# Optimization experiments

Hardware: AMD Instinct MI355X
Metric: run time of the kernel (lower is better)

## Reference

```python
import jax, jax.numpy as jnp
import numpy as np

DIM, HEADS, RANK = 768, 12, 64
HEAD_DIM = DIM // HEADS

def _xavier(key, shape):
    fan_in, fan_out = shape[1], shape[0]
    std = (2.0 / (fan_in + fan_out)) ** 0.5
    return std * jax.random.normal(key, shape, dtype=jnp.float32)

def setup_inputs() -> dict:
    key = jax.random.key(0)
    ks = jax.random.split(key, 12)
    B, N = 8, 1024
    x = jax.random.normal(ks[0], (B, N, DIM), dtype=jnp.float32)
    params = {}
    for i, nm in enumerate(['Q', 'K', 'V']):
        params[f'W_{nm}0'] = _xavier(ks[1 + 3 * i], (DIM, RANK))
        params[f'W_{nm}1'] = _xavier(ks[2 + 3 * i], (HEADS, RANK))
        params[f'W_{nm}2'] = _xavier(ks[3 + 3 * i], (HEAD_DIM, RANK))
    proj_w = _xavier(ks[10], (DIM, DIM))
    proj_b = jnp.zeros((DIM,), dtype=jnp.float32)
    return dict(x=x, W_Q0=params['W_Q0'], W_Q1=params['W_Q1'], W_Q2=params['W_Q2'],
                W_K0=params['W_K0'], W_K1=params['W_K1'], W_K2=params['W_K2'],
                W_V0=params['W_V0'], W_V1=params['W_V1'], W_V2=params['W_V2'],
                proj_w=proj_w, proj_b=proj_b)

def _cp_proj(xh, W2, W1, W0, B, N, H, hd):
    # xh: [B,N,H,hd]; contract head_dim with W2 and heads with W1 -> [B,N,R], then expand to dim via W0
    t = jnp.einsum('blnd,dr,nr->blr', xh, W2, W1)
    out = jnp.einsum('blr,mr->blm', t, W0)          # [B,N,dim]
    return out.reshape(B, N, H, hd).transpose(0, 2, 1, 3)  # [B,H,N,hd]

def reference(x, W_Q0, W_Q1, W_Q2, W_K0, W_K1, W_K2, W_V0, W_V1, W_V2, proj_w, proj_b):
    B, N, C = x.shape
    H = W_Q1.shape[0]
    hd = C // H
    scale = hd ** -0.5
    xh = x.reshape(B, N, H, hd)
    q = _cp_proj(xh, W_Q2, W_Q1, W_Q0, B, N, H, hd)
    k = _cp_proj(xh, W_K2, W_K1, W_K0, B, N, H, hd)
    v = _cp_proj(xh, W_V2, W_V1, W_V0, B, N, H, hd)
    attn = jax.nn.softmax(jnp.einsum('bhqd,bhkd->bhqk', q, k) * scale, axis=-1)
    out = jnp.einsum('bhqk,bhkd->bhqd', attn, v).transpose(0, 2, 1, 3).reshape(B, N, C)
    return out @ proj_w.T + proj_b
```

## Files before the change

### kernel.cpp

```cpp
#include <hip/hip_runtime.h>

typedef unsigned short u16;
typedef __attribute__((ext_vector_type(8))) short bf16x8;
typedef __attribute__((ext_vector_type(4))) float f32x4;
typedef __attribute__((ext_vector_type(4))) unsigned short u16x4;
typedef __attribute__((ext_vector_type(8))) unsigned short u16x8;

#define AS1 __attribute__((address_space(1)))
#define AS3 __attribute__((address_space(3)))

__device__ __forceinline__ float b2f(u16 s) {
    return __uint_as_float(((unsigned)s) << 16);
}
__device__ __forceinline__ u16 f2b(float f) {
    unsigned u = __float_as_uint(f);
    unsigned r = 0x7fffu + ((u >> 16) & 1u);
    return (u16)((u + r) >> 16);
}

__device__ __forceinline__ unsigned packtrunc(float p0, float p1) {
#if __has_builtin(__builtin_amdgcn_perm)
    return __builtin_amdgcn_perm(__float_as_uint(p1), __float_as_uint(p0), 0x07060302u);
#else
    return (__float_as_uint(p0) >> 16) | (__float_as_uint(p1) & 0xffff0000u);
#endif
}

__device__ __forceinline__ void g2l16(const u16* g, u16* l) {
    __builtin_amdgcn_global_load_lds((const AS1 void*)g, (AS3 void*)l, 16, 0, 0);
}

#if __has_builtin(__builtin_amdgcn_exp2f)
#define EXP2(x) __builtin_amdgcn_exp2f(x)
#else
#define EXP2(x) exp2f(x)
#endif

__global__ __launch_bounds__(256, 2) void fused_t_prep(
    const float* __restrict__ X,
    const float* __restrict__ Wq0, const float* __restrict__ Wq1, const float* __restrict__ Wq2,
    const float* __restrict__ Wk0, const float* __restrict__ Wk1, const float* __restrict__ Wk2,
    const float* __restrict__ Wv0, const float* __restrict__ Wv1, const float* __restrict__ Wv2,
    const float* __restrict__ PW,
    u16* __restrict__ T, u16* __restrict__ tvt,
    u16* __restrict__ MqkT, u16* __restrict__ Dcat)
{
    __shared__ __align__(16) char smem[33280];
    const int bx = blockIdx.x;
    const int t = threadIdx.x;

    if (bx < 384) {
        u16*   As  = (u16*)smem;
        u16*   Bs  = (u16*)(smem + 4096);
        float* W1t = (float*)(smem + 8192);
        float* W2t = (float*)(smem + 11264);

        const int lane = t & 63, wv = t >> 6;
        const int l15 = lane & 15, quad = lane >> 4;

        const int lin = bx;
        const int xcd = lin & 7, j = lin >> 3;
        const int col = j % 3, rowhi = j / 3;
        const int rowBase = (rowhi * 8 + xcd) * 64;
        const int colBase = col * 64;

        const float* W1g = (col == 0) ? Wq1 : (col == 1) ? Wk1 : Wv1;
        const float* W2g = (col == 0) ? Wq2 : (col == 1) ? Wk2 : Wv2;
        for (int i = t; i < 768; i += 256) W1t[i] = W1g[i];
        for (int i = t; i < 4096; i += 256) {
            const int d = i >> 6, r = i & 63;
            W2t[r * 65 + d] = W2g[i];
        }

        const int srow = t >> 2;
        const int scol = (t & 3) * 8;
        const float* aS = X + (size_t)(rowBase + srow) * 768 + scol;

        float4 a0 = *(const float4*)(aS);
        float4 a1 = *(const float4*)(aS + 4);

        const f32x4 zero4 = {0.f, 0.f, 0.f, 0.f};
        f32x4 acc[4];
#pragma unroll
        for (int tn = 0; tn < 4; ++tn) acc[tn] = zero4;

        for (int kk = 0; kk < 768; kk += 32) {
            __syncthreads();
            u16x8 ap;
            ap[0] = f2b(a0.x); ap[1] = f2b(a0.y); ap[2] = f2b(a0.z); ap[3] = f2b(a0.w);
            ap[4] = f2b(a1.x); ap[5] = f2b(a1.y); ap[6] = f2b(a1.z); ap[7] = f2b(a1.w);
            *(u16x8*)&As[srow * 32 + scol] = ap;
            {
                const int c0 = kk + scol;
                const int hh = c0 >> 6, dd = c0 & 63;
                const float w1v = W1t[hh * 64 + srow];
                u16x8 bp;
#pragma unroll
                for (int jj = 0; jj < 8; ++jj)
                    bp[jj] = f2b(w1v * W2t[srow * 65 + dd + jj]);
                *(u16x8*)&Bs[srow * 32 + scol] = bp;
            }
            __syncthreads();

            if (kk < 736) {
                a0 = *(const float4*)(aS + kk + 32);
                a1 = *(const float4*)(aS + kk + 36);
            }

            const bf16x8 af = *(const bf16x8*)(As + (wv * 16 + l15) * 32 + quad * 8);
#pragma unroll
            for (int tn = 0; tn < 4; ++tn) {
                const bf16x8 bf = *(const bf16x8*)(Bs + (tn * 16 + l15) * 32 + quad * 8);
                acc[tn] = __builtin_amdgcn_mfma_f32_16x16x32_bf16(af, bf, acc[tn], 0, 0, 0);
            }
        }

        if (colBase < 128) {
#pragma unroll
            for (int tn = 0; tn < 4; ++tn) {
                const int c = colBase + tn * 16 + l15;
#pragma unroll
                for (int r = 0; r < 4; ++r) {
                    const int grow = rowBase + wv * 16 + quad * 4 + r;
                    T[(size_t)grow * 128 + c] = f2b(acc[tn][r]);
                }
            }
        } else {
#pragma unroll
            for (int tn = 0; tn < 4; ++tn) {
                const int rr = tn * 16 + l15;
                const int grow = rowBase + wv * 16 + quad * 4;
                u16x4 pk;
                pk.x = f2b(acc[tn][0]); pk.y = f2b(acc[tn][1]);
                pk.z = f2b(acc[tn][2]); pk.w = f2b(acc[tn][3]);
                *(u16x4*)(tvt + (size_t)rr * 8192 + grow) = pk;
            }
        }
    } else if (bx < 432) {
        float* wq = (float*)smem;
        float* wk = (float*)(smem + 16640);
        const int hq = bx - 384;
        const int h = hq >> 2, quarter = hq & 3;
        const float qs = 0.125f * 1.4426950408889634f;
        for (int i = t; i < 4096; i += 256) {
            const int dd = i >> 6, r = i & 63;
            wq[dd * 65 + r] = Wq0[(h * 64 + dd) * 64 + r] * qs;
            wk[dd * 65 + r] = Wk0[(h * 64 + dd) * 64 + r];
        }
        __syncthreads();
        const int j0 = quarter * 1024 + t * 4;
        const int r2 = j0 >> 6, r1b = j0 & 63;
        u16x4 pk;
#pragma unroll
        for (int jj = 0; jj < 4; ++jj) {
            float acc = 0.f;
#pragma unroll
            for (int dd = 0; dd < 64; ++dd)
                acc += wk[dd * 65 + r2] * wq[dd * 65 + r1b + jj];
            ((u16*)&pk)[jj] = f2b(acc);
        }
        *(u16x4*)(MqkT + (size_t)(h * 64 + r2) * 64 + r1b) = pk;
    } else {
        float* w0s = (float*)smem;
        float* pws = (float*)(smem + 16640);
        const int hb = bx - 432;
        const int h = hb / 24, mBase = (hb - h * 24) * 32;
        for (int i = t; i < 4096; i += 256) {
            const int d = i >> 6, r = i & 63;
            w0s[d * 65 + r] = Wv0[(h * 64 + d) * 64 + r];
        }
        for (int i = t; i < 2048; i += 256) {
            const int mi = i >> 6, d = i & 63;
            pws[mi * 65 + d] = PW[(size_t)(mBase + mi) * 768 + h * 64 + d];
        }
        __syncthreads();
        const int r = t & 63, mi0 = t >> 6;
        float w0c[64];
#pragma unroll
        for (int d = 0; d < 64; ++d) w0c[d] = w0s[d * 65 + r];
        for (int mi = mi0; mi < 32; mi += 4) {
            float acc = 0.f;
#pragma unroll
            for (int d = 0; d < 64; ++d) acc += pws[mi * 65 + d] * w0c[d];
            Dcat[(size_t)(mBase + mi) * 768 + h * 64 + r] = f2b(acc);
        }
    }
}

__global__ __launch_bounds__(256, 3) void flash_attn10(
    const u16* __restrict__ T, const u16* __restrict__ MqkT,
    const u16* __restrict__ tvt, u16* __restrict__ Z)
{
    const int bh = blockIdx.x;
    const int qt = blockIdx.y;
    const int b = bh / 12, h = bh - b * 12;
    const u16* qp = T + ((size_t)b * 1024 + qt * 128) * 128;
    const u16* kp = T + (size_t)b * 1024 * 128 + 64;
    const u16* vp = tvt + b * 1024;

    __shared__ u16 B0raw[2 * 64 * 72];
    __shared__ u16 B1raw[2 * 64 * 72];

    const int t = threadIdx.x;
    const int lane = t & 63, wv = t >> 6;
    const int l15 = lane & 15, quad = lane >> 4;

    bf16x8 qf[2][2];
#pragma unroll
    for (int qg = 0; qg < 2; ++qg) {
        const u16* qrow = qp + (size_t)(wv * 32 + qg * 16 + l15) * 128;
        qf[qg][0] = *(const bf16x8*)(qrow + quad * 8);
        qf[qg][1] = *(const bf16x8*)(qrow + 32 + quad * 8);
    }

    const int srow = t >> 2;
    const int scol = (t & 3) * 16;
    const int p5 = srow & 31;
    const int lrow = (srow & 32) | ((p5 & 4) << 2) | ((p5 & 16) >> 1)
                   | ((p5 & 8) >> 1) | (p5 & 3);

    bf16x8 vone = {};
    if (l15 == 0) {
#pragma unroll
        for (int j = 0; j < 8; ++j) vone[j] = (short)0x3F80;
    }

    int4 kr0 = *(const int4*)(kp + (size_t)srow * 128 + scol);
    int4 kr1 = *(const int4*)(kp + (size_t)srow * 128 + scol + 8);
    int4 vr0 = *(const int4*)(vp + (size_t)srow * 8192 + scol);
    int4 vr1 = *(const int4*)(vp + (size_t)srow * 8192 + scol + 8);

    const f32x4 zero4 = {0.f, 0.f, 0.f, 0.f};
    {
        f32x4 Wt[2][4];
#pragma unroll
        for (int qg = 0; qg < 2; ++qg)
#pragma unroll
            for (int tn = 0; tn < 4; ++tn) Wt[qg][tn] = zero4;
#pragma unroll
        for (int ks = 0; ks < 2; ++ks) {
#pragma unroll
            for (int tn = 0; tn < 4; ++tn) {
                const bf16x8 mb = *(const bf16x8*)(
                    MqkT + (size_t)(h * 64 + tn * 16 + l15) * 64 + ks * 32 + quad * 8);
                Wt[0][tn] = __builtin_amdgcn_mfma_f32_16x16x32_bf16(qf[0][ks], mb, Wt[0][tn], 0, 0, 0);
                Wt[1][tn] = __builtin_amdgcn_mfma_f32_16x16x32_bf16(qf[1][ks], mb, Wt[1][tn], 0, 0, 0);
            }
        }
#pragma unroll
        for (int qg = 0; qg < 2; ++qg)
#pragma unroll
            for (int tn = 0; tn < 4; ++tn)
#pragma unroll
                for (int r = 0; r < 4; ++r)
                    B1raw[(wv * 32 + qg * 16 + quad * 4 + r) * 72 + tn * 16 + l15] =
                        f2b(Wt[qg][tn][r]);
    }
    __syncthreads();
    bf16x8 wf[2][2];
#pragma unroll
    for (int qg = 0; qg < 2; ++qg) {
        wf[qg][0] = *(const bf16x8*)&B1raw[(wv * 32 + qg * 16 + l15) * 72 + quad * 8];
        wf[qg][1] = *(const bf16x8*)&B1raw[(wv * 32 + qg * 16 + l15) * 72 + 32 + quad * 8];
    }

    *(int4*)&B0raw[lrow * 72 + scol]                 = kr0;
    *(int4*)&B0raw[lrow * 72 + scol + 8]             = kr1;
    *(int4*)&B0raw[64 * 72 + srow * 72 + scol]       = vr0;
    *(int4*)&B0raw[64 * 72 + srow * 72 + scol + 8]   = vr1;
    kr0 = *(const int4*)(kp + (size_t)(64 + srow) * 128 + scol);
    kr1 = *(const int4*)(kp + (size_t)(64 + srow) * 128 + scol + 8);
    vr0 = *(const int4*)(vp + (size_t)srow * 8192 + 64 + scol);
    vr1 = *(const int4*)(vp + (size_t)srow * 8192 + 64 + scol + 8);
    __syncthreads();

    f32x4 o_acc[2][4];
    f32x4 Lacc[2] = {zero4, zero4};
#pragma unroll
    for (int qg = 0; qg < 2; ++qg)
#pragma unroll
        for (int tn = 0; tn < 4; ++tn) o_acc[qg][tn] = zero4;

#define STAGE(NB)                                                               \
    {                                                                           \
        *(int4*)&NB[lrow * 72 + scol]               = kr0;                      \
        *(int4*)&NB[lrow * 72 + scol + 8]           = kr1;                      \
        *(int4*)&NB[64 * 72 + srow * 72 + scol]     = vr0;                      \
        *(int4*)&NB[64 * 72 + srow * 72 + scol + 8] = vr1;                      \
    }
#define PREFETCH(KT)                                                            \
    {                                                                           \
        kr0 = *(const int4*)(kp + (size_t)((KT) * 64 + srow) * 128 + scol);     \
        kr1 = *(const int4*)(kp + (size_t)((KT) * 64 + srow) * 128 + scol + 8); \
        vr0 = *(const int4*)(vp + (size_t)srow * 8192 + (KT) * 64 + scol);      \
        vr1 = *(const int4*)(vp + (size_t)srow * 8192 + (KT) * 64 + scol + 8);  \
    }
#define FLASH_TILE(KB)                                                          \
    {                                                                           \
        f32x4 Sacc[2][4];                                                       \
        _Pragma("unroll")                                                       \
        for (int qg = 0; qg < 2; ++qg)                                          \
            _Pragma("unroll")                                                   \
            for (int tk = 0; tk < 4; ++tk) Sacc[qg][tk] = zero4;                \
        _Pragma("unroll")                                                       \
        for (int ks = 0; ks < 2; ++ks) {                                        \
            _Pragma("unroll")                                                   \
            for (int tk = 0; tk < 4; ++tk) {                                    \
                const bf16x8 kf = *(const bf16x8*)&KB[(tk * 16 + l15) * 72 + ks * 32 + quad * 8]; \
                Sacc[0][tk] = __builtin_amdgcn_mfma_f32_16x16x32_bf16(kf, wf[0][ks], Sacc[0][tk], 0, 0, 0); \
                Sacc[1][tk] = __builtin_amdgcn_mfma_f32_16x16x32_bf16(kf, wf[1][ks], Sacc[1][tk], 0, 0, 0); \
            }                                                                   \
        }                                                                       \
        union { bf16x8 v; unsigned u[4]; } pf[2][2];                            \
        _Pragma("unroll")                                                       \
        for (int qg = 0; qg < 2; ++qg)                                          \
            _Pragma("unroll")                                                   \
            for (int tk = 0; tk < 4; ++tk) {                                    \
                const float p0 = EXP2(Sacc[qg][tk][0]);                         \
                const float p1 = EXP2(Sacc[qg][tk][1]);                         \
                const float p2 = EXP2(Sacc[qg][tk][2]);                         \
                const float p3 = EXP2(Sacc[qg][tk][3]);                         \
                const int g = tk >> 1, hf = (tk & 1) * 2;                       \
                pf[qg][g].u[hf + 0] = packtrunc(p0, p1);                        \
                pf[qg][g].u[hf + 1] = packtrunc(p2, p3);                        \
            }                                                                   \
        _Pragma("unroll")                                                       \
        for (int g = 0; g < 2; ++g) {                                           \
            _Pragma("unroll")                                                   \
            for (int tn = 0; tn < 4; ++tn) {                                    \
                const bf16x8 vf = *(const bf16x8*)&KB[64 * 72 + (tn * 16 + l15) * 72 + g * 32 + quad * 8]; \
                o_acc[0][tn] = __builtin_amdgcn_mfma_f32_16x16x32_bf16(pf[0][g].v, vf, o_acc[0][tn], 0, 0, 0); \
                o_acc[1][tn] = __builtin_amdgcn_mfma_f32_16x16x32_bf16(pf[1][g].v, vf, o_acc[1][tn], 0, 0, 0); \
            }                                                                   \
            Lacc[0] = __builtin_amdgcn_mfma_f32_16x16x32_bf16(pf[0][g].v, vone, Lacc[0], 0, 0, 0); \
            Lacc[1] = __builtin_amdgcn_mfma_f32_16x16x32_bf16(pf[1][g].v, vone, Lacc[1], 0, 0, 0); \
        }                                                                       \
    }

    for (int t8 = 0; t8 < 8; ++t8) {
        const int kt0 = 2 * t8;
        STAGE(B1raw);
        if (t8 < 7) PREFETCH(kt0 + 2);
        FLASH_TILE(B0raw);
        __syncthreads();
        if (t8 < 7) {
            STAGE(B0raw);
            PREFETCH(kt0 + 3);
        }
        FLASH_TILE(B1raw);
        if (t8 < 7) __syncthreads();
    }

#undef STAGE
#undef PREFETCH
#undef FLASH_TILE

#pragma unroll
    for (int qg = 0; qg < 2; ++qg) {
#pragma unroll
        for (int r = 0; r < 4; ++r) {
            const float Lv = __shfl(Lacc[qg][r], quad << 4, 64);
            const float inv = 1.0f / Lv;
            const int token = qt * 128 + wv * 32 + qg * 16 + quad * 4 + r;
#pragma unroll
            for (int tn = 0; tn < 4; ++tn) {
                const int col = h * 64 + tn * 16 + l15;
                Z[(size_t)(b * 1024 + token) * 768 + col] = f2b(o_acc[qg][tn][r] * inv);
            }
        }
    }
}

__global__ __launch_bounds__(256, 3) void gemm_out(
    const u16* __restrict__ A, const u16* __restrict__ Bt,
    float* __restrict__ C, const float* __restrict__ bias)
{
    __shared__ u16 As[128 * 32];
    __shared__ u16 Bs[64 * 32];

    const int tid  = threadIdx.x;
    const int lane = tid & 63, wv = tid >> 6;
    const int l15  = lane & 15, quad = lane >> 4;

    const int lin = blockIdx.x + 12 * blockIdx.y;
    const int xcd = lin & 7, j = lin >> 3;
    const int colT = j % 12, rowhi = j / 12;
    const int rowBase = (rowhi * 8 + xcd) * 128;
    const int colBase = colT * 64;

    const int srowA = wv * 32 + (lane >> 2);
    const int srowB = wv * 16 + (lane >> 2);
    const int scol  = (lane & 3) * 8;
    const u16* aSrc = A  + (size_t)(rowBase + srowA) * 768 + scol;
    const u16* bSrc = Bt + (size_t)(colBase + srowB) * 768 + scol;
    u16* aDst = As + wv * 1024;
    u16* bDst = Bs + wv * 512;

    const f32x4 zero4 = {0.f, 0.f, 0.f, 0.f};
    f32x4 acc[2][4];
#pragma unroll
    for (int tm = 0; tm < 2; ++tm)
#pragma unroll
        for (int tn = 0; tn < 4; ++tn) acc[tm][tn] = zero4;

    for (int kk = 0; kk < 768; kk += 32) {
        __syncthreads();
        g2l16(aSrc + kk,            aDst);
        g2l16(aSrc + kk + 16 * 768, aDst + 512);
        g2l16(bSrc + kk,            bDst);
        __syncthreads();

        bf16x8 af[2], bfm[4];
#pragma unroll
        for (int t = 0; t < 2; ++t)
            af[t]  = *(const bf16x8*)(As + (wv * 32 + t * 16 + l15) * 32 + quad * 8);
#pragma unroll
        for (int t = 0; t < 4; ++t)
            bfm[t] = *(const bf16x8*)(Bs + (t * 16 + l15) * 32 + quad * 8);
#pragma unroll
        for (int tm = 0; tm < 2; ++tm)
#pragma unroll
            for (int tn = 0; tn < 4; ++tn)
                acc[tm][tn] = __builtin_amdgcn_mfma_f32_16x16x32_bf16(
                    af[tm], bfm[tn], acc[tm][tn], 0, 0, 0);
    }

#pragma unroll
    for (int tm = 0; tm < 2; ++tm) {
        const int grow = rowBase + wv * 32 + tm * 16 + quad * 4;
#pragma unroll
        for (int tn = 0; tn < 4; ++tn) {
            const int gcol = colBase + tn * 16 + l15;
            const float bv = bias[gcol];
#pragma unroll
            for (int r = 0; r < 4; ++r)
                C[(size_t)(grow + r) * 768 + gcol] = acc[tm][tn][r] + bv;
        }
    }
}

extern "C" void kernel_launch(void* const* d_in, const int* in_sizes, int n_in,
                              void* d_out, int out_size, void* d_ws, size_t ws_size,
                              hipStream_t stream)
{
    const float* x      = (const float*)d_in[0];
    const float* Wq0    = (const float*)d_in[1];
    const float* Wq1    = (const float*)d_in[2];
    const float* Wq2    = (const float*)d_in[3];
    const float* Wk0    = (const float*)d_in[4];
    const float* Wk1    = (const float*)d_in[5];
    const float* Wk2    = (const float*)d_in[6];
    const float* Wv0    = (const float*)d_in[7];
    const float* Wv1    = (const float*)d_in[8];
    const float* Wv2    = (const float*)d_in[9];
    const float* proj_w = (const float*)d_in[10];
    const float* proj_b = (const float*)d_in[11];
    float* outp = (float*)d_out;

    char* ws = (char*)d_ws;
    u16* T    = (u16*)ws;
    u16* tvt  = (u16*)(ws + 2097152);
    u16* MqkT = (u16*)(ws + 3440640);
    u16* Dcat = (u16*)(ws + 3538944);
    u16* Zcat = (u16*)(ws + 4718592);

    fused_t_prep<<<720, 256, 0, stream>>>(x, Wq0, Wq1, Wq2, Wk0, Wk1, Wk2,
                                          Wv0, Wv1, Wv2, proj_w,
                                          T, tvt, MqkT, Dcat);
    flash_attn10<<<dim3(96, 8), 256, 0, stream>>>(T, MqkT, tvt, Zcat);
    gemm_out<<<dim3(12, 64), 256, 0, stream>>>(Zcat, Dcat, outp, proj_b);
}
```

Measured before the change: 163.1 us.

## Fuse three kernels into one persistent launch with software grid barriers

Merges the prep, flash-attention and output-GEMM kernels into a single 768-block kernel that separates the phases with atomic-counter grid barriers. It falls back to three separate launches when the occupancy query reports fewer than three resident blocks per CU. The aim is to remove the launch gaps and tail drain between kernels. In exchange, all phases share one register and LDS budget under launch_bounds(256,3), the barriers add spin-wait cost, and correctness depends on all 768 blocks being co-resident.

```diff
diff --git a/kernel.cpp b/kernel.cpp
--- a/kernel.cpp
+++ b/kernel.cpp
@@ -9,9 +9,6 @@
 #define AS1 __attribute__((address_space(1)))
 #define AS3 __attribute__((address_space(3)))
 
-__device__ __forceinline__ float b2f(u16 s) {
-    return __uint_as_float(((unsigned)s) << 16);
-}
 __device__ __forceinline__ u16 f2b(float f) {
     unsigned u = __float_as_uint(f);
     unsigned r = 0x7fffu + ((u >> 16) & 1u);
@@ -36,7 +33,38 @@
 #define EXP2(x) exp2f(x)
 #endif
 
-__global__ __launch_bounds__(256, 2) void fused_t_prep(
+__device__ unsigned g_cnt[2];
+__device__ unsigned g_gen[2];
+
+__device__ __forceinline__ void gbar(int i, unsigned nblk) {
+    __syncthreads();
+    if (threadIdx.x == 0) {
+        __threadfence();
+        const unsigned my = __hip_atomic_load(&g_gen[i], __ATOMIC_RELAXED,
+                                              __HIP_MEMORY_SCOPE_AGENT);
+        const unsigned v = __hip_atomic_fetch_add(&g_cnt[i], 1u, __ATOMIC_ACQ_REL,
+                                                  __HIP_MEMORY_SCOPE_AGENT);
+        if (v == nblk - 1u) {
+            __hip_atomic_store(&g_cnt[i], 0u, __ATOMIC_RELAXED,
+                               __HIP_MEMORY_SCOPE_AGENT);
+            __threadfence();
+            __hip_atomic_fetch_add(&g_gen[i], 1u, __ATOMIC_ACQ_REL,
+                                   __HIP_MEMORY_SCOPE_AGENT);
+        } else {
+            unsigned spins = 0;
+            while (__hip_atomic_load(&g_gen[i], __ATOMIC_ACQUIRE,
+                                     __HIP_MEMORY_SCOPE_AGENT) == my) {
+                __builtin_amdgcn_s_sleep(2);
+                if (++spins > (1u << 22)) break;
+            }
+        }
+        __threadfence();
+    }
+    __syncthreads();
+}
+
+__device__ __forceinline__ void phaseA(
+    const int bid, const int t, char* smem,
     const float* __restrict__ X,
     const float* __restrict__ Wq0, const float* __restrict__ Wq1, const float* __restrict__ Wq2,
     const float* __restrict__ Wk0, const float* __restrict__ Wk1, const float* __restrict__ Wk2,
@@ -45,11 +73,8 @@
     u16* __restrict__ T, u16* __restrict__ tvt,
     u16* __restrict__ MqkT, u16* __restrict__ Dcat)
 {
-    __shared__ __align__(16) char smem[33280];
-    const int bx = blockIdx.x;
-    const int t = threadIdx.x;
-
-    if (bx < 384) {
+    const f32x4 zero4 = {0.f, 0.f, 0.f, 0.f};
+    if (bid < 384) {
         u16*   As  = (u16*)smem;
         u16*   Bs  = (u16*)(smem + 4096);
         float* W1t = (float*)(smem + 8192);
@@ -58,7 +83,7 @@
         const int lane = t & 63, wv = t >> 6;
         const int l15 = lane & 15, quad = lane >> 4;
 
-        const int lin = bx;
+        const int lin = bid;
         const int xcd = lin & 7, j = lin >> 3;
         const int col = j % 3, rowhi = j / 3;
         const int rowBase = (rowhi * 8 + xcd) * 64;
@@ -79,7 +104,6 @@
         float4 a0 = *(const float4*)(aS);
         float4 a1 = *(const float4*)(aS + 4);
 
-        const f32x4 zero4 = {0.f, 0.f, 0.f, 0.f};
         f32x4 acc[4];
 #pragma unroll
         for (int tn = 0; tn < 4; ++tn) acc[tn] = zero4;
@@ -136,10 +160,10 @@
                 *(u16x4*)(tvt + (size_t)rr * 8192 + grow) = pk;
             }
         }
-    } else if (bx < 432) {
+    } else if (bid < 432) {
         float* wq = (float*)smem;
         float* wk = (float*)(smem + 16640);
-        const int hq = bx - 384;
+        const int hq = bid - 384;
         const int h = hq >> 2, quarter = hq & 3;
         const float qs = 0.125f * 1.4426950408889634f;
         for (int i = t; i < 4096; i += 256) {
@@ -160,10 +184,10 @@
             ((u16*)&pk)[jj] = f2b(acc);
         }
         *(u16x4*)(MqkT + (size_t)(h * 64 + r2) * 64 + r1b) = pk;
-    } else {
+    } else if (bid < 720) {
         float* w0s = (float*)smem;
         float* pws = (float*)(smem + 16640);
-        const int hb = bx - 432;
+        const int hb = bid - 432;
         const int h = hb / 24, mBase = (hb - h * 24) * 32;
         for (int i = t; i < 4096; i += 256) {
             const int d = i >> 6, r = i & 63;
@@ -187,23 +211,24 @@
     }
 }
 
-__global__ __launch_bounds__(256, 3) void flash_attn10(
+__device__ __forceinline__ void phaseB(
+    const int bid, const int t, char* smem,
     const u16* __restrict__ T, const u16* __restrict__ MqkT,
-    const u16* __restrict__ tvt, u16* __restrict__ Z)
-{
-    const int bh = blockIdx.x;
-    const int qt = blockIdx.y;
+    const u16* __restrict__ tvt, u16* __restrict__ Zcat)
+{
+    const int bh = bid % 96;
+    const int qt = bid / 96;
     const int b = bh / 12, h = bh - b * 12;
     const u16* qp = T + ((size_t)b * 1024 + qt * 128) * 128;
     const u16* kp = T + (size_t)b * 1024 * 128 + 64;
     const u16* vp = tvt + b * 1024;
 
-    __shared__ u16 B0raw[2 * 64 * 72];
-    __shared__ u16 B1raw[2 * 64 * 72];
-
-    const int t = threadIdx.x;
+    u16* const B0raw = (u16*)smem;
+    u16* const B1raw = (u16*)(smem + 18432);
+
     const int lane = t & 63, wv = t >> 6;
     const int l15 = lane & 15, quad = lane >> 4;
+    const f32x4 zero4 = {0.f, 0.f, 0.f, 0.f};
 
     bf16x8 qf[2][2];
 #pragma unroll
@@ -230,7 +255,6 @@
     int4 vr0 = *(const int4*)(vp + (size_t)srow * 8192 + scol);
     int4 vr1 = *(const int4*)(vp + (size_t)srow * 8192 + scol + 8);
 
-    const f32x4 zero4 = {0.f, 0.f, 0.f, 0.f};
     {
         f32x4 Wt[2][4];
 #pragma unroll
@@ -365,24 +389,25 @@
 #pragma unroll
             for (int tn = 0; tn < 4; ++tn) {
                 const int col = h * 64 + tn * 16 + l15;
-                Z[(size_t)(b * 1024 + token) * 768 + col] = f2b(o_acc[qg][tn][r] * inv);
-            }
-        }
-    }
-}
-
-__global__ __launch_bounds__(256, 3) void gemm_out(
-    const u16* __restrict__ A, const u16* __restrict__ Bt,
-    float* __restrict__ C, const float* __restrict__ bias)
-{
-    __shared__ u16 As[128 * 32];
-    __shared__ u16 Bs[64 * 32];
-
-    const int tid  = threadIdx.x;
-    const int lane = tid & 63, wv = tid >> 6;
-    const int l15  = lane & 15, quad = lane >> 4;
-
-    const int lin = blockIdx.x + 12 * blockIdx.y;
+                Zcat[(size_t)(b * 1024 + token) * 768 + col] = f2b(o_acc[qg][tn][r] * inv);
+            }
+        }
+    }
+}
+
+__device__ __forceinline__ void phaseC(
+    const int bid, const int t, char* smem,
+    const u16* __restrict__ Zcat, const u16* __restrict__ Dcat,
+    float* __restrict__ outp, const float* __restrict__ bias)
+{
+    u16* As = (u16*)smem;
+    u16* Bs = (u16*)(smem + 8192);
+
+    const int lane = t & 63, wv = t >> 6;
+    const int l15 = lane & 15, quad = lane >> 4;
+    const f32x4 zero4 = {0.f, 0.f, 0.f, 0.f};
+
+    const int lin = bid;
     const int xcd = lin & 7, j = lin >> 3;
     const int colT = j % 12, rowhi = j / 12;
     const int rowBase = (rowhi * 8 + xcd) * 128;
@@ -391,12 +416,11 @@
     const int srowA = wv * 32 + (lane >> 2);
     const int srowB = wv * 16 + (lane >> 2);
     const int scol  = (lane & 3) * 8;
-    const u16* aSrc = A  + (size_t)(rowBase + srowA) * 768 + scol;
-    const u16* bSrc = Bt + (size_t)(colBase + srowB) * 768 + scol;
+    const u16* aSrc = Zcat + (size_t)(rowBase + srowA) * 768 + scol;
+    const u16* bSrc = Dcat + (size_t)(colBase + srowB) * 768 + scol;
     u16* aDst = As + wv * 1024;
     u16* bDst = Bs + wv * 512;
 
-    const f32x4 zero4 = {0.f, 0.f, 0.f, 0.f};
     f32x4 acc[2][4];
 #pragma unroll
     for (int tm = 0; tm < 2; ++tm)
@@ -412,11 +436,11 @@
 
         bf16x8 af[2], bfm[4];
 #pragma unroll
-        for (int t = 0; t < 2; ++t)
-            af[t]  = *(const bf16x8*)(As + (wv * 32 + t * 16 + l15) * 32 + quad * 8);
-#pragma unroll
-        for (int t = 0; t < 4; ++t)
-            bfm[t] = *(const bf16x8*)(Bs + (t * 16 + l15) * 32 + quad * 8);
+        for (int tt = 0; tt < 2; ++tt)
+            af[tt]  = *(const bf16x8*)(As + (wv * 32 + tt * 16 + l15) * 32 + quad * 8);
+#pragma unroll
+        for (int tt = 0; tt < 4; ++tt)
+            bfm[tt] = *(const bf16x8*)(Bs + (tt * 16 + l15) * 32 + quad * 8);
 #pragma unroll
         for (int tm = 0; tm < 2; ++tm)
 #pragma unroll
@@ -434,9 +458,60 @@
             const float bv = bias[gcol];
 #pragma unroll
             for (int r = 0; r < 4; ++r)
-                C[(size_t)(grow + r) * 768 + gcol] = acc[tm][tn][r] + bv;
-        }
-    }
+                outp[(size_t)(grow + r) * 768 + gcol] = acc[tm][tn][r] + bv;
+        }
+    }
+}
+
+__global__ __launch_bounds__(256, 3) void mega(
+    const float* __restrict__ X,
+    const float* __restrict__ Wq0, const float* __restrict__ Wq1, const float* __restrict__ Wq2,
+    const float* __restrict__ Wk0, const float* __restrict__ Wk1, const float* __restrict__ Wk2,
+    const float* __restrict__ Wv0, const float* __restrict__ Wv1, const float* __restrict__ Wv2,
+    const float* __restrict__ PW, const float* __restrict__ bias,
+    u16* __restrict__ T, u16* __restrict__ tvt,
+    u16* __restrict__ MqkT, u16* __restrict__ Dcat,
+    u16* __restrict__ Zcat, float* __restrict__ outp)
+{
+    __shared__ __align__(16) char smem[36864];
+    const int bid = blockIdx.x, t = threadIdx.x;
+    if (bid < 720)
+        phaseA(bid, t, smem, X, Wq0, Wq1, Wq2, Wk0, Wk1, Wk2, Wv0, Wv1, Wv2, PW,
+               T, tvt, MqkT, Dcat);
+    gbar(0, 768u);
+    phaseB(bid, t, smem, T, MqkT, tvt, Zcat);
+    gbar(1, 768u);
+    phaseC(bid, t, smem, Zcat, Dcat, outp, bias);
+}
+
+__global__ __launch_bounds__(256, 2) void k_prep(
+    const float* __restrict__ X,
+    const float* __restrict__ Wq0, const float* __restrict__ Wq1, const float* __restrict__ Wq2,
+    const float* __restrict__ Wk0, const float* __restrict__ Wk1, const float* __restrict__ Wk2,
+    const float* __restrict__ Wv0, const float* __restrict__ Wv1, const float* __restrict__ Wv2,
+    const float* __restrict__ PW,
+    u16* __restrict__ T, u16* __restrict__ tvt,
+    u16* __restrict__ MqkT, u16* __restrict__ Dcat)
+{
+    __shared__ __align__(16) char smem[36864];
+    phaseA(blockIdx.x, threadIdx.x, smem, X, Wq0, Wq1, Wq2, Wk0, Wk1, Wk2,
+           Wv0, Wv1, Wv2, PW, T, tvt, MqkT, Dcat);
+}
+
+__global__ __launch_bounds__(256, 3) void k_flash(
+    const u16* __restrict__ T, const u16* __restrict__ MqkT,
+    const u16* __restrict__ tvt, u16* __restrict__ Zcat)
+{
+    __shared__ __align__(16) char smem[36864];
+    phaseB(blockIdx.x + 96 * blockIdx.y, threadIdx.x, smem, T, MqkT, tvt, Zcat);
+}
+
+__global__ __launch_bounds__(256, 3) void k_out(
+    const u16* __restrict__ Zcat, const u16* __restrict__ Dcat,
+    float* __restrict__ outp, const float* __restrict__ bias)
+{
+    __shared__ __align__(16) char smem[36864];
+    phaseC(blockIdx.x, threadIdx.x, smem, Zcat, Dcat, outp, bias);
 }
 
 extern "C" void kernel_launch(void* const* d_in, const int* in_sizes, int n_in,
@@ -464,9 +539,22 @@
     u16* Dcat = (u16*)(ws + 3538944);
     u16* Zcat = (u16*)(ws + 4718592);
 
-    fused_t_prep<<<720, 256, 0, stream>>>(x, Wq0, Wq1, Wq2, Wk0, Wk1, Wk2,
-                                          Wv0, Wv1, Wv2, proj_w,
-                                          T, tvt, MqkT, Dcat);
-    flash_attn10<<<dim3(96, 8), 256, 0, stream>>>(T, MqkT, tvt, Zcat);
-    gemm_out<<<dim3(12, 64), 256, 0, stream>>>(Zcat, Dcat, outp, proj_b);
-}
+    static int use_mega = -1;
+    if (use_mega < 0) {
+        int nb = 0;
+        hipError_t e = hipOccupancyMaxActiveBlocksPerMultiprocessor(&nb, mega, 256, 0);
+        use_mega = (e == hipSuccess && nb >= 3) ? 1 : 0;
+    }
+
+    if (use_mega) {
+        mega<<<768, 256, 0, stream>>>(x, Wq0, Wq1, Wq2, Wk0, Wk1, Wk2,
+                                      Wv0, Wv1, Wv2, proj_w, proj_b,
+                                      T, tvt, MqkT, Dcat, Zcat, outp);
+    } else {
+        k_prep<<<720, 256, 0, stream>>>(x, Wq0, Wq1, Wq2, Wk0, Wk1, Wk2,
+                                        Wv0, Wv1, Wv2, proj_w,
+                                        T, tvt, MqkT, Dcat);
+        k_flash<<<dim3(96, 8), 256, 0, stream>>>(T, MqkT, tvt, Zcat);
+        k_out<<<768, 256, 0, stream>>>(Zcat, Dcat, outp, proj_b);
+    }
+}
```

Measured after the change: 165.3 us. No clear change (+1.3%).
